# Kernel optimization log

Hardware: AMD Instinct MI355X
Metric: run time of the kernel (lower is better)

The kernel has to match this reference:

```python
import jax, jax.numpy as jnp
import numpy as np

B, M, GRID = 4, 8192, 32          # batches, points per batch, voxel grid side
N = B * M
K = 8                              # knn neighbors (includes self at dist 0)
C_IN, C_OUT, H = 8, 8, 128
KEYB = 64                          # hash base (coords shifted +1 stay in [0,33])
EPS = 1e-5


def setup_inputs() -> dict:
    rng = np.random.default_rng(0)
    # unique occupied voxels per batch (ME SparseTensor requires unique coords)
    cs = []
    for b in range(B):
        lin = rng.choice(GRID ** 3, size=M, replace=False)
        x, y, z = lin // (GRID * GRID), (lin // GRID) % GRID, lin % GRID
        cs.append(np.stack([np.full(M, b), x, y, z], axis=1))
    coords = jnp.asarray(np.concatenate(cs, axis=0).astype(np.int32))  # [N,4]

    key = jax.random.key(0)
    ks = jax.random.split(key, 4)
    feats = jax.random.normal(ks[0], (N, C_IN), jnp.float32)
    w1 = jax.random.normal(ks[1], ((K + 1) * C_IN, H), jnp.float32) * 0.05  # 1x1 conv
    g1 = jnp.ones((H,), jnp.float32)
    b1 = jnp.zeros((H,), jnp.float32)
    w3 = jax.random.normal(ks[2], (27, H, H), jnp.float32) * 0.02          # 3^3 sparse conv
    g2 = jnp.ones((H,), jnp.float32)
    b2 = jnp.zeros((H,), jnp.float32)
    w_out = jax.random.normal(ks[3], (H, 2 * C_OUT), jnp.float32) * 0.05   # 1x1 conv
    return dict(coords=coords, feats=feats, w1=w1, g1=g1, b1=b1,
                w3=w3, g2=g2, b2=b2, w_out=w_out)


def _knn_idx(coords):
    # per-batch brute-force kNN on xyz (batch column segments the search)
    xyz = coords[:, 1:].astype(jnp.float32).reshape(B, M, 3)
    d2 = jnp.sum((xyz[:, :, None, :] - xyz[:, None, :, :]) ** 2, -1)  # [B,M,M]
    _, idx = jax.lax.top_k(-d2, K)                                     # [B,M,K]
    return (idx + (jnp.arange(B) * M)[:, None, None]).reshape(N, K)


def _bn(x, g, b):
    mu = jnp.mean(x, axis=0)
    var = jnp.var(x, axis=0)
    return (x - mu) * jax.lax.rsqrt(var + EPS) * g + b


def reference(coords, feats, w1, g1, b1, w3, g2, b2, w_out):
    # --- kNN gather-and-build: [center || k neighbor feats] -> (k+1)*C_in ---
    nbr = _knn_idx(coords)                                        # [N,K] int
    combined = jnp.concatenate([feats[:, None, :], feats[nbr]], axis=1)
    combined = combined.reshape(N, (K + 1) * C_IN)
    # --- neighbor_processor: 1x1 conv + BN + ReLU ---
    h = jax.nn.relu(_bn(combined @ w1, g1, b1))                   # [N,H]
    # --- context_predictor conv k=3: gather inputs at coord+offset via hash ---
    c = coords[:, 1:] + 1                                         # shift so offsets stay >= 0
    keys = ((coords[:, 0] * KEYB + c[:, 0]) * KEYB + c[:, 1]) * KEYB + c[:, 2]
    order = jnp.argsort(keys)
    skeys = keys[order]
    offs = jnp.stack(jnp.meshgrid(*([jnp.arange(-1, 2)] * 3), indexing='ij'),
                     axis=-1).reshape(27, 3)                      # {-1,0,1}^3
    okey = (offs[:, 0] * KEYB + offs[:, 1]) * KEYB + offs[:, 2]   # [27]
    q = keys[None, :] + okey[:, None]                             # [27,N]
    pos = jnp.clip(jnp.searchsorted(skeys, q), 0, N - 1)
    valid = skeys[pos] == q                                       # [27,N]
    j = order[pos]                                                # [27,N]
    gathered = jnp.where(valid[..., None], h[j], 0.0)             # [27,N,H]
    h2 = jnp.einsum('onc,ocd->nd', gathered, w3)                  # [N,H]
    h2 = jax.nn.relu(_bn(h2, g2, b2))
    # --- final 1x1 conv -> mean/scale ---
    return h2 @ w_out                                             # [N, 2*C_OUT]
```

## Files before the change

kernel.cpp:

```cpp
#include <hip/hip_runtime.h>
#include <hip/hip_bf16.h>

#define B_   4
#define M_   8192
#define N_   32768
#define H_   128
#define EPS_ 1e-5f
#define TBL  1048576
#define GUARD 8192

typedef short short8 __attribute__((ext_vector_type(8)));
typedef float f32x4  __attribute__((ext_vector_type(4)));

__global__ __launch_bounds__(256) void prep_kernel(const int* __restrict__ coords,
                                                   int* __restrict__ table,
                                                   int* __restrict__ packed,
                                                   int* __restrict__ keyb,
                                                   float* __restrict__ gsum,
                                                   unsigned int* __restrict__ hbz) {
    int n = blockIdx.x * 256 + threadIdx.x;
    int b = coords[4*n+0], x = coords[4*n+1], y = coords[4*n+2], z = coords[4*n+3];
    packed[n] = (x << 10) | (y << 5) | z;
    int key = ((b*64 + x+1)*64 + y+1)*64 + (z+1);
    keyb[n] = key;
    table[key] = n;
    if (blockIdx.x == 0) gsum[threadIdx.x] = 0.f;
    if (blockIdx.x == 1 && threadIdx.x < 64) hbz[threadIdx.x] = 0u;
}

__global__ __launch_bounds__(256) void w3pack_kernel(const float* __restrict__ w3,
                                                     ushort* __restrict__ w3f) {
    int t = blockIdx.x * 256 + threadIdx.x;
    int lane = t & 63;
    int ct   = (t >> 6) & 7;
    int ks   = (t >> 9) & 3;
    int o    = t >> 11;
    int quad = lane >> 4, l15 = lane & 15;
    int n = ct*16 + l15;
    const float* src = w3 + o*16384;
    ushort out8[8];
#pragma unroll
    for (int j = 0; j < 8; ++j) {
        int c = ks*32 + quad*8 + j;
        float v = src[c*128 + n];
        __hip_bfloat16 bv = __float2bfloat16(v);
        ushort u; __builtin_memcpy(&u, &bv, 2);
        out8[j] = u;
    }
    *(uint4*)&w3f[t*8] = *(uint4*)out8;
}

__global__ __launch_bounds__(256) void knn_window_kernel(const int* __restrict__ table,
                                                         const int* __restrict__ keyb,
                                                         int* __restrict__ nbr,
                                                         int* __restrict__ flagcnt,
                                                         int* __restrict__ flaglist) {
    __shared__ int okey_sh[125], d2_sh[125];
    __shared__ int tops[256 * 8];
    int tid = threadIdx.x;
    if (tid < 125) {
        int dx = tid / 25 - 2, rr = tid % 25, dy = rr / 5 - 2, dz = rr % 5 - 2;
        okey_sh[tid] = dx * 4096 + dy * 64 + dz;
        d2_sh[tid]   = dx*dx + dy*dy + dz*dz;
    }
    __syncthreads();

    int q   = blockIdx.x * 64 + (tid >> 2);
    int sub = tid & 3;
    int kb  = keyb[q];

    int top[8];
#pragma unroll
    for (int k = 0; k < 8; ++k) top[k] = 0x7FFFFFFF;

    int base = sub * 32;
    int cnt  = (sub == 3) ? 29 : 32;
    for (int i = 0; i < cnt; ++i) {
        int idx = base + i;
        int j = table[kb + okey_sh[idx]];
        if (j >= 0) {
            int key = (d2_sh[idx] << 13) | (j & 8191);
            if (key < top[7]) {
#pragma unroll
                for (int k = 7; k >= 1; --k)
                    top[k] = (key < top[k]) ? max(key, top[k-1]) : top[k];
                top[0] = min(key, top[0]);
            }
        }
    }
#pragma unroll
    for (int k = 0; k < 8; ++k) tops[tid*8 + k] = top[k];
    __syncthreads();

    if (sub == 0) {
        const int* L = &tops[tid*8];
        int ia0 = 0, ia1 = 0, ia2 = 0, ia3 = 0;
        int res[8];
#pragma unroll
        for (int k = 0; k < 8; ++k) {
            int v0 = L[ia0], v1 = L[8 + ia1], v2 = L[16 + ia2], v3 = L[24 + ia3];
            int m01 = min(v0, v1), m23 = min(v2, v3);
            int m = min(m01, m23);
            res[k] = m;
            if (m == v0) ++ia0; else if (m == v1) ++ia1;
            else if (m == v2) ++ia2; else ++ia3;
        }
        int bb = q & ~(M_-1);
        if ((res[7] >> 13) <= 8) {
#pragma unroll
            for (int k = 0; k < 8; ++k) nbr[q*8 + k] = bb + (res[k] & 8191);
        } else {
            int pos = atomicAdd(flagcnt, 1);
            flaglist[pos] = q;
        }
    }
}

__global__ __launch_bounds__(256) void knn_bf_kernel(const int* __restrict__ packed,
                                                     const int* __restrict__ flagcnt,
                                                     const int* __restrict__ flaglist,
                                                     int* __restrict__ nbr) {
    __shared__ int tops[256 * 8];
    int tid = threadIdx.x;
    int cnt = *flagcnt;
    for (int f = blockIdx.x; f < cnt; f += gridDim.x) {
        int n = flaglist[f];
        int bb = n & ~(M_-1);
        int p = packed[n];
        int qx = (p >> 10) & 31, qy = (p >> 5) & 31, qz = p & 31;
        int top[8];
#pragma unroll
        for (int k = 0; k < 8; ++k) top[k] = 0x7FFFFFFF;
        for (int j = tid; j < M_; j += 256) {
            int c = packed[bb + j];
            int dx = qx - ((c >> 10) & 31);
            int dy = qy - ((c >> 5) & 31);
            int dz = qz - (c & 31);
            int d2 = dx*dx + dy*dy + dz*dz;
            int key = (d2 << 13) | j;
            if (key < top[7]) {
#pragma unroll
                for (int k = 7; k >= 1; --k)
                    top[k] = (key < top[k]) ? max(key, top[k-1]) : top[k];
                top[0] = min(key, top[0]);
            }
        }
#pragma unroll
        for (int k = 0; k < 8; ++k) tops[tid*8 + k] = top[k];
        __syncthreads();
        for (int stride = 128; stride >= 1; stride >>= 1) {
            if (tid < stride) {
                int* A  = &tops[tid*8];
                int* Bp = &tops[(tid+stride)*8];
                int r[8]; int ia = 0, ib = 0;
#pragma unroll
                for (int k = 0; k < 8; ++k) {
                    int a = A[ia], b2 = Bp[ib];
                    if (a <= b2) { r[k] = a; ++ia; } else { r[k] = b2; ++ib; }
                }
#pragma unroll
                for (int k = 0; k < 8; ++k) A[k] = r[k];
            }
            __syncthreads();
        }
        if (tid == 0) {
#pragma unroll
            for (int k = 0; k < 8; ++k) nbr[n*8 + k] = bb + (tops[k] & 8191);
        }
        __syncthreads();
    }
}

__global__ __launch_bounds__(256) void h1_kernel(const float* __restrict__ feats,
                                                 const int* __restrict__ nbr,
                                                 const float* __restrict__ w1,
                                                 float* __restrict__ hpre) {
    __shared__ float comb[16][72];
    int tid = threadIdx.x;
    int rowbase = blockIdx.x * 16;
    if (tid < 144) {
        int r = tid / 9, s = tid % 9;
        int grow = rowbase + r;
        int idx = (s == 0) ? grow : nbr[grow*8 + (s-1)];
        const float4* f = (const float4*)(feats + idx * 8);
        float4 a = f[0], b = f[1];
        float* dp = &comb[r][s*8];
        dp[0]=a.x; dp[1]=a.y; dp[2]=a.z; dp[3]=a.w;
        dp[4]=b.x; dp[5]=b.y; dp[6]=b.z; dp[7]=b.w;
    }
    __syncthreads();
    int c = tid & 127, rh = tid >> 7;
    float acc[8];
#pragma unroll
    for (int i = 0; i < 8; ++i) acc[i] = 0.f;
    for (int s = 0; s < 72; ++s) {
        float w = w1[s*128 + c];
#pragma unroll
        for (int i = 0; i < 8; ++i)
            acc[i] += comb[rh*8 + i][s] * w;
    }
#pragma unroll
    for (int i = 0; i < 8; ++i)
        hpre[(rowbase + rh*8 + i)*128 + c] = acc[i];
}

__global__ __launch_bounds__(256) void reduce_kernel(const float* __restrict__ src,
                                                     float* __restrict__ part) {
    __shared__ float ssum[256], ssq[256];
    int tid = threadIdx.x;
    int c = tid & 127, halfr = tid >> 7;
    int rowbase = blockIdx.x * 128 + halfr * 64;
    float s = 0.f, q = 0.f;
    for (int i = 0; i < 64; ++i) {
        float v = src[(rowbase + i)*128 + c];
        s += v; q += v*v;
    }
    ssum[tid] = s; ssq[tid] = q;
    __syncthreads();
    if (tid < 128) {
        part[blockIdx.x*256 + tid]       = ssum[tid] + ssum[tid+128];
        part[blockIdx.x*256 + 128 + tid] = ssq[tid]  + ssq[tid+128];
    }
}

__global__ __launch_bounds__(128) void stats_kernel(const float* __restrict__ part,
                                                    const float* __restrict__ g,
                                                    const float* __restrict__ bias,
                                                    float* __restrict__ scale,
                                                    float* __restrict__ shift) {
    int c = threadIdx.x;
    float s = 0.f, q = 0.f;
    for (int b = 0; b < 256; ++b) {
        s += part[b*256 + c];
        q += part[b*256 + 128 + c];
    }
    float mu  = s / (float)N_;
    float var = q / (float)N_ - mu*mu;
    float inv = rsqrtf(var + EPS_);
    float sc  = inv * g[c];
    scale[c] = sc;
    shift[c] = bias[c] - mu * sc;
}

__global__ __launch_bounds__(128) void stats2_kernel(const float* __restrict__ gsum,
                                                     const float* __restrict__ g,
                                                     const float* __restrict__ bias,
                                                     float* __restrict__ scale,
                                                     float* __restrict__ shift) {
    int c = threadIdx.x;
    float s = gsum[c], q = gsum[128 + c];
    float mu  = s / (float)N_;
    float var = q / (float)N_ - mu*mu;
    float inv = rsqrtf(var + EPS_);
    float sc  = inv * g[c];
    scale[c] = sc;
    shift[c] = bias[c] - mu * sc;
}

__global__ __launch_bounds__(256) void bnrelu_bf16_kernel(const float* __restrict__ x,
                                                          const float* __restrict__ scale,
                                                          const float* __restrict__ shift,
                                                          ushort* __restrict__ y) {
    int i = blockIdx.x * 256 + threadIdx.x;
    float4 v = ((const float4*)x)[i];
    int c = (i * 4) & 127;
    v.x = fmaxf(0.f, v.x*scale[c]   + shift[c]);
    v.y = fmaxf(0.f, v.y*scale[c+1] + shift[c+1]);
    v.z = fmaxf(0.f, v.z*scale[c+2] + shift[c+2]);
    v.w = fmaxf(0.f, v.w*scale[c+3] + shift[c+3]);
    ushort o[4];
#pragma unroll
    for (int k = 0; k < 4; ++k) {
        float f = (&v.x)[k];
        __hip_bfloat16 bv = __float2bfloat16(f);
        __builtin_memcpy(&o[k], &bv, 2);
    }
    ((ushort4*)y)[i] = make_ushort4(o[0], o[1], o[2], o[3]);
}

#define CONV3_LDS 145408
__global__ __launch_bounds__(512) void conv3_mfma_kernel(const ushort* __restrict__ hb,
                                                         const ushort* __restrict__ w3f,
                                                         const int* __restrict__ table,
                                                         const int* __restrict__ keyb,
                                                         float* __restrict__ h2,
                                                         float* __restrict__ gsum) {
    extern __shared__ char smem_raw[];
    ushort* Asb = (ushort*)smem_raw;
    ushort* Bsb = (ushort*)(smem_raw + 65536);
    int*    jsh = (int*)(smem_raw + 131072);
    int*    kbsh= (int*)(smem_raw + 144896);

    int tid = threadIdx.x;
    int lane = tid & 63, wid = tid >> 6;
    int quad = lane >> 4, l15 = lane & 15;
    int bid = blockIdx.x;
    int swz = (bid & 7) * 32 + (bid >> 3);
    int rowbase = swz * 128;
    int wr = wid >> 1;
    int cb = (wid & 1) * 4;

    if (tid < 128) kbsh[tid] = keyb[rowbase + tid];
    __syncthreads();
    for (int t = tid; t < 27*128; t += 512) {
        int o = t >> 7, r = t & 127;
        int dx = o/9 - 1, dy = (o/3)%3 - 1, dz = o%3 - 1;
        jsh[t] = table[kbsh[r] + dx*4096 + dy*64 + dz];
    }
    __syncthreads();

#pragma unroll
    for (int i = 0; i < 4; ++i) {
        int flat = i*512 + tid;
        int r = flat >> 4, cp = flat & 15;
        int j = jsh[r];
        const ushort* asrc = hb + j*128 + ((cp ^ (r & 15)) << 3);
        __builtin_amdgcn_global_load_lds(
            (const __attribute__((address_space(1))) unsigned int*)asrc,
            (__attribute__((address_space(3))) unsigned int*)&Asb[flat << 3],
            16, 0, 0);
        __builtin_amdgcn_global_load_lds(
            (const __attribute__((address_space(1))) unsigned int*)(w3f + (flat << 3)),
            (__attribute__((address_space(3))) unsigned int*)&Bsb[flat << 3],
            16, 0, 0);
    }
    __syncthreads();

    f32x4 acc[2][4];
#pragma unroll
    for (int i = 0; i < 2; ++i)
#pragma unroll
        for (int c = 0; c < 4; ++c)
            acc[i][c] = (f32x4){0.f, 0.f, 0.f, 0.f};

    int cur = 0;
#pragma unroll 1
    for (int o = 0; o < 27; ++o) {
        if (o < 26) {
            int obase = (o + 1) << 7;
            const ushort* wsrc = w3f + ((o + 1) << 14);
            int dst = (cur ^ 1) * 16384;
#pragma unroll
            for (int i = 0; i < 4; ++i) {
                int flat = i*512 + tid;
                int r = flat >> 4, cp = flat & 15;
                int j = jsh[obase + r];
                const ushort* asrc = hb + j*128 + ((cp ^ (r & 15)) << 3);
                __builtin_amdgcn_global_load_lds(
                    (const __attribute__((address_space(1))) unsigned int*)asrc,
                    (__attribute__((address_space(3))) unsigned int*)&Asb[dst + (flat << 3)],
                    16, 0, 0);
                __builtin_amdgcn_global_load_lds(
                    (const __attribute__((address_space(1))) unsigned int*)(wsrc + (flat << 3)),
                    (__attribute__((address_space(3))) unsigned int*)&Bsb[dst + (flat << 3)],
                    16, 0, 0);
            }
        }
        const ushort* Ac = Asb + cur*16384;
        const ushort* Bc = Bsb + cur*16384;
#pragma unroll
        for (int ks = 0; ks < 4; ++ks) {
            short8 af[2], bfr[4];
#pragma unroll
            for (int i = 0; i < 2; ++i) {
                int lr = wr*32 + i*16 + l15;
                int chunk = (ks*4 + quad) ^ l15;
                af[i] = *(const short8*)&Ac[lr*128 + chunk*8];
            }
#pragma unroll
            for (int c = 0; c < 4; ++c)
                bfr[c] = *(const short8*)&Bc[((ks*8 + cb + c)*64 + lane) << 3];
#pragma unroll
            for (int i = 0; i < 2; ++i)
#pragma unroll
                for (int c = 0; c < 4; ++c)
                    acc[i][c] = __builtin_amdgcn_mfma_f32_16x16x32_bf16(af[i], bfr[c], acc[i][c], 0, 0, 0);
        }
        __syncthreads();
        cur ^= 1;
    }

    float s[4], q[4];
#pragma unroll
    for (int c = 0; c < 4; ++c) { s[c] = 0.f; q[c] = 0.f; }
#pragma unroll
    for (int i = 0; i < 2; ++i)
#pragma unroll
        for (int c = 0; c < 4; ++c)
#pragma unroll
            for (int r = 0; r < 4; ++r) {
                int row = rowbase + wr*32 + i*16 + quad*4 + r;
                int col = (cb + c)*16 + l15;
                float v = acc[i][c][r];
                h2[row*128 + col] = v;
                s[c] += v; q[c] += v*v;
            }
    float* red = (float*)smem_raw;
    if (tid < 256) red[tid] = 0.f;
    __syncthreads();
#pragma unroll
    for (int c = 0; c < 4; ++c) {
        int col = (cb + c)*16 + l15;
        atomicAdd(&red[col], s[c]);
        atomicAdd(&red[128 + col], q[c]);
    }
    __syncthreads();
    if (tid < 256) atomicAdd(&gsum[tid], red[tid]);
}

__global__ __launch_bounds__(256) void out_kernel(const float* __restrict__ h2,
                                                  const float* __restrict__ wout,
                                                  const float* __restrict__ scale,
                                                  const float* __restrict__ shift,
                                                  float* __restrict__ out) {
    __shared__ float sc[128], sh[128];
    int tid = threadIdx.x;
    if (tid < 128) { sc[tid] = scale[tid]; sh[tid] = shift[tid]; }
    __syncthreads();
    int r = tid >> 4, d = tid & 15;
    int row = blockIdx.x * 16 + r;
    float acc = 0.f;
    for (int c = 0; c < 128; ++c) {
        float hv = fmaxf(0.f, fmaf(h2[row*128 + c], sc[c], sh[c]));
        acc = fmaf(hv, wout[c*16 + d], acc);
    }
    out[row*16 + d] = acc;
}

extern "C" void kernel_launch(void* const* d_in, const int* in_sizes, int n_in,
                              void* d_out, int out_size, void* d_ws, size_t ws_size,
                              hipStream_t stream) {
    const int*   coords = (const int*)d_in[0];
    const float* feats  = (const float*)d_in[1];
    const float* w1     = (const float*)d_in[2];
    const float* g1     = (const float*)d_in[3];
    const float* b1     = (const float*)d_in[4];
    const float* w3     = (const float*)d_in[5];
    const float* g2     = (const float*)d_in[6];
    const float* b2     = (const float*)d_in[7];
    const float* wout   = (const float*)d_in[8];
    float* out = (float*)d_out;

    char* ws = (char*)d_ws;
    int*    table_base = (int*)(ws);
    int*    table   = table_base + GUARD;
    int*    packed  = (int*)(ws + (4352u<<10));
    int*    keyb    = (int*)(ws + (4608u<<10));
    int*    nbr     = (int*)(ws + (4864u<<10));
    int*    flagcnt = (int*)(ws + (5888u<<10));
    int*    flaglist= (int*)(ws + (5892u<<10));
    float*  part    = (float*)(ws + (6144u<<10));
    float*  scale1  = (float*)(ws + (6400u<<10));
    float*  shift1  = scale1 + 128;
    float*  scale2  = shift1 + 128;
    float*  shift2  = scale2 + 128;
    float*  gsum    = (float*)(ws + (6416u<<10));
    ushort* w3f     = (ushort*)(ws + (6656u<<10));
    ushort* hb      = (ushort*)(ws + (7680u<<10));
    float*  h       = (float*)(ws + (15872u<<10));
    float*  h2      = h;

    static bool conv3_attr_set = false;
    if (!conv3_attr_set) {
        hipFuncSetAttribute(reinterpret_cast<const void*>(&conv3_mfma_kernel),
                            hipFuncAttributeMaxDynamicSharedMemorySize, CONV3_LDS);
        conv3_attr_set = true;
    }

    hipMemsetAsync(table_base, 0xFF, (TBL + GUARD) * sizeof(int), stream);
    hipMemsetAsync(flagcnt, 0, sizeof(int), stream);
    prep_kernel      <<<N_/256, 256, 0, stream>>>(coords, table, packed, keyb,
                                                  gsum, (unsigned int*)(hb - 128));
    w3pack_kernel    <<<216, 256, 0, stream>>>(w3, w3f);
    knn_window_kernel<<<N_/64, 256, 0, stream>>>(table, keyb, nbr, flagcnt, flaglist);
    knn_bf_kernel    <<<256, 256, 0, stream>>>(packed, flagcnt, flaglist, nbr);
    h1_kernel        <<<N_/16, 256, 0, stream>>>(feats, nbr, w1, h);
    reduce_kernel    <<<N_/128, 256, 0, stream>>>(h, part);
    stats_kernel     <<<1, 128, 0, stream>>>(part, g1, b1, scale1, shift1);
    bnrelu_bf16_kernel<<<(N_*H_/4)/256, 256, 0, stream>>>(h, scale1, shift1, hb);
    conv3_mfma_kernel<<<N_/128, 512, CONV3_LDS, stream>>>(hb, w3f, table, keyb, h2, gsum);
    stats2_kernel    <<<1, 128, 0, stream>>>(gsum, g2, b2, scale2, shift2);
    out_kernel       <<<N_/16, 256, 0, stream>>>(h2, wout, scale2, shift2, out);
}
```

Before: 228.4 us.

## Fuse BN statistics into producers, merge prep kernels, prune kNN window

Merges prep and w3 packing into one launch and moves the flag-counter reset there, replacing a memset. BN1 sum and sum-of-squares are now accumulated in h1_kernel with atomics into 8 slots, so the separate reduce pass over h disappears. The stats kernels are folded into bnrelu and out_kernel, which each recompute scale and shift per block. The kNN window now probes only offsets with squared distance at most 8 instead of the full 5x5x5 cube. out_kernel is rebuilt to stage 128 rows and the output weights in LDS with vectorised loads. These changes cut launches and an extra full read of h. The cost is atomic contention, redundant per-block stats work, and kNN correctness resting on the brute-force fallback catching points the smaller window misses.

```diff
diff --git a/kernel.cpp b/kernel.cpp
--- a/kernel.cpp
+++ b/kernel.cpp
@@ -12,25 +12,31 @@
 typedef short short8 __attribute__((ext_vector_type(8)));
 typedef float f32x4  __attribute__((ext_vector_type(4)));
 
-__global__ __launch_bounds__(256) void prep_kernel(const int* __restrict__ coords,
-                                                   int* __restrict__ table,
-                                                   int* __restrict__ packed,
-                                                   int* __restrict__ keyb,
-                                                   float* __restrict__ gsum,
-                                                   unsigned int* __restrict__ hbz) {
-    int n = blockIdx.x * 256 + threadIdx.x;
-    int b = coords[4*n+0], x = coords[4*n+1], y = coords[4*n+2], z = coords[4*n+3];
-    packed[n] = (x << 10) | (y << 5) | z;
-    int key = ((b*64 + x+1)*64 + y+1)*64 + (z+1);
-    keyb[n] = key;
-    table[key] = n;
-    if (blockIdx.x == 0) gsum[threadIdx.x] = 0.f;
-    if (blockIdx.x == 1 && threadIdx.x < 64) hbz[threadIdx.x] = 0u;
-}
-
-__global__ __launch_bounds__(256) void w3pack_kernel(const float* __restrict__ w3,
-                                                     ushort* __restrict__ w3f) {
-    int t = blockIdx.x * 256 + threadIdx.x;
+__global__ __launch_bounds__(256) void prep_pack_kernel(const int* __restrict__ coords,
+                                                        int* __restrict__ table,
+                                                        int* __restrict__ packed,
+                                                        int* __restrict__ keyb,
+                                                        const float* __restrict__ w3,
+                                                        ushort* __restrict__ w3f,
+                                                        float* __restrict__ gsum1,
+                                                        float* __restrict__ gsum2,
+                                                        int* __restrict__ flagcnt,
+                                                        unsigned int* __restrict__ hbz) {
+    int bid = blockIdx.x, tid = threadIdx.x;
+    if (bid < 128) {
+        int n = bid * 256 + tid;
+        int b = coords[4*n+0], x = coords[4*n+1], y = coords[4*n+2], z = coords[4*n+3];
+        packed[n] = (x << 10) | (y << 5) | z;
+        int key = ((b*64 + x+1)*64 + y+1)*64 + (z+1);
+        keyb[n] = key;
+        table[key] = n;
+        if (bid < 8)  gsum1[bid*256 + tid] = 0.f;
+        if (bid == 0) gsum2[tid] = 0.f;
+        if (bid == 8 && tid < 64) hbz[tid] = 0u;
+        if (bid == 9 && tid == 0) *flagcnt = 0;
+        return;
+    }
+    int t = (bid - 128) * 256 + tid;
     int lane = t & 63;
     int ct   = (t >> 6) & 7;
     int ks   = (t >> 9) & 3;
@@ -55,13 +61,20 @@
                                                          int* __restrict__ nbr,
                                                          int* __restrict__ flagcnt,
                                                          int* __restrict__ flaglist) {
-    __shared__ int okey_sh[125], d2_sh[125];
+    __shared__ int okey_sh[93], d2_sh[93];
     __shared__ int tops[256 * 8];
+    __shared__ int ncnt;
     int tid = threadIdx.x;
+    if (tid == 0) ncnt = 0;
+    __syncthreads();
     if (tid < 125) {
         int dx = tid / 25 - 2, rr = tid % 25, dy = rr / 5 - 2, dz = rr % 5 - 2;
-        okey_sh[tid] = dx * 4096 + dy * 64 + dz;
-        d2_sh[tid]   = dx*dx + dy*dy + dz*dz;
+        int d2 = dx*dx + dy*dy + dz*dz;
+        if (d2 <= 8) {
+            int p = atomicAdd(&ncnt, 1);
+            okey_sh[p] = dx * 4096 + dy * 64 + dz;
+            d2_sh[p]   = d2;
+        }
     }
     __syncthreads();
 
@@ -73,8 +86,8 @@
 #pragma unroll
     for (int k = 0; k < 8; ++k) top[k] = 0x7FFFFFFF;
 
-    int base = sub * 32;
-    int cnt  = (sub == 3) ? 29 : 32;
+    int base = sub * 24;
+    int cnt  = (sub == 3) ? 21 : 24;
     for (int i = 0; i < cnt; ++i) {
         int idx = base + i;
         int j = table[kb + okey_sh[idx]];
@@ -174,8 +187,10 @@
 __global__ __launch_bounds__(256) void h1_kernel(const float* __restrict__ feats,
                                                  const int* __restrict__ nbr,
                                                  const float* __restrict__ w1,
-                                                 float* __restrict__ hpre) {
+                                                 float* __restrict__ hpre,
+                                                 float* __restrict__ gsum1) {
     __shared__ float comb[16][72];
+    __shared__ float ssum[256], ssq[256];
     int tid = threadIdx.x;
     int rowbase = blockIdx.x * 16;
     if (tid < 144) {
@@ -199,75 +214,52 @@
         for (int i = 0; i < 8; ++i)
             acc[i] += comb[rh*8 + i][s] * w;
     }
-#pragma unroll
-    for (int i = 0; i < 8; ++i)
+    float s = 0.f, q = 0.f;
+#pragma unroll
+    for (int i = 0; i < 8; ++i) {
         hpre[(rowbase + rh*8 + i)*128 + c] = acc[i];
-}
-
-__global__ __launch_bounds__(256) void reduce_kernel(const float* __restrict__ src,
-                                                     float* __restrict__ part) {
-    __shared__ float ssum[256], ssq[256];
+        s += acc[i]; q += acc[i]*acc[i];
+    }
+    ssum[tid] = s; ssq[tid] = q;
+    __syncthreads();
+    if (tid < 128) {
+        float S = ssum[tid] + ssum[tid+128];
+        float Q = ssq[tid]  + ssq[tid+128];
+        float* g = gsum1 + (blockIdx.x & 7) * 256;
+        atomicAdd(&g[tid], S);
+        atomicAdd(&g[128 + tid], Q);
+    }
+}
+
+__global__ __launch_bounds__(256) void bnrelu_bf16_kernel(const float* __restrict__ x,
+                                                          const float* __restrict__ gsum1,
+                                                          const float* __restrict__ g1,
+                                                          const float* __restrict__ b1,
+                                                          ushort* __restrict__ y) {
+    __shared__ float sc[128], sh[128];
     int tid = threadIdx.x;
-    int c = tid & 127, halfr = tid >> 7;
-    int rowbase = blockIdx.x * 128 + halfr * 64;
-    float s = 0.f, q = 0.f;
-    for (int i = 0; i < 64; ++i) {
-        float v = src[(rowbase + i)*128 + c];
-        s += v; q += v*v;
-    }
-    ssum[tid] = s; ssq[tid] = q;
-    __syncthreads();
     if (tid < 128) {
-        part[blockIdx.x*256 + tid]       = ssum[tid] + ssum[tid+128];
-        part[blockIdx.x*256 + 128 + tid] = ssq[tid]  + ssq[tid+128];
-    }
-}
-
-__global__ __launch_bounds__(128) void stats_kernel(const float* __restrict__ part,
-                                                    const float* __restrict__ g,
-                                                    const float* __restrict__ bias,
-                                                    float* __restrict__ scale,
-                                                    float* __restrict__ shift) {
-    int c = threadIdx.x;
-    float s = 0.f, q = 0.f;
-    for (int b = 0; b < 256; ++b) {
-        s += part[b*256 + c];
-        q += part[b*256 + 128 + c];
-    }
-    float mu  = s / (float)N_;
-    float var = q / (float)N_ - mu*mu;
-    float inv = rsqrtf(var + EPS_);
-    float sc  = inv * g[c];
-    scale[c] = sc;
-    shift[c] = bias[c] - mu * sc;
-}
-
-__global__ __launch_bounds__(128) void stats2_kernel(const float* __restrict__ gsum,
-                                                     const float* __restrict__ g,
-                                                     const float* __restrict__ bias,
-                                                     float* __restrict__ scale,
-                                                     float* __restrict__ shift) {
-    int c = threadIdx.x;
-    float s = gsum[c], q = gsum[128 + c];
-    float mu  = s / (float)N_;
-    float var = q / (float)N_ - mu*mu;
-    float inv = rsqrtf(var + EPS_);
-    float sc  = inv * g[c];
-    scale[c] = sc;
-    shift[c] = bias[c] - mu * sc;
-}
-
-__global__ __launch_bounds__(256) void bnrelu_bf16_kernel(const float* __restrict__ x,
-                                                          const float* __restrict__ scale,
-                                                          const float* __restrict__ shift,
-                                                          ushort* __restrict__ y) {
-    int i = blockIdx.x * 256 + threadIdx.x;
+        float s = 0.f, q = 0.f;
+#pragma unroll
+        for (int r = 0; r < 8; ++r) {
+            s += gsum1[r*256 + tid];
+            q += gsum1[r*256 + 128 + tid];
+        }
+        float mu  = s / (float)N_;
+        float var = q / (float)N_ - mu*mu;
+        float inv = rsqrtf(var + EPS_);
+        float scv = inv * g1[tid];
+        sc[tid] = scv;
+        sh[tid] = b1[tid] - mu * scv;
+    }
+    __syncthreads();
+    int i = blockIdx.x * 256 + tid;
     float4 v = ((const float4*)x)[i];
     int c = (i * 4) & 127;
-    v.x = fmaxf(0.f, v.x*scale[c]   + shift[c]);
-    v.y = fmaxf(0.f, v.y*scale[c+1] + shift[c+1]);
-    v.z = fmaxf(0.f, v.z*scale[c+2] + shift[c+2]);
-    v.w = fmaxf(0.f, v.w*scale[c+3] + shift[c+3]);
+    v.x = fmaxf(0.f, v.x*sc[c]   + sh[c]);
+    v.y = fmaxf(0.f, v.y*sc[c+1] + sh[c+1]);
+    v.z = fmaxf(0.f, v.z*sc[c+2] + sh[c+2]);
+    v.w = fmaxf(0.f, v.w*sc[c+3] + sh[c+3]);
     ushort o[4];
 #pragma unroll
     for (int k = 0; k < 4; ++k) {
@@ -410,21 +402,62 @@
 
 __global__ __launch_bounds__(256) void out_kernel(const float* __restrict__ h2,
                                                   const float* __restrict__ wout,
-                                                  const float* __restrict__ scale,
-                                                  const float* __restrict__ shift,
+                                                  const float* __restrict__ gsum2,
+                                                  const float* __restrict__ g2,
+                                                  const float* __restrict__ b2,
                                                   float* __restrict__ out) {
+    __shared__ float hrow[128][129];
+    __shared__ float wsh[2048];
     __shared__ float sc[128], sh[128];
     int tid = threadIdx.x;
-    if (tid < 128) { sc[tid] = scale[tid]; sh[tid] = shift[tid]; }
-    __syncthreads();
-    int r = tid >> 4, d = tid & 15;
-    int row = blockIdx.x * 16 + r;
-    float acc = 0.f;
+    if (tid < 128) {
+        float s = gsum2[tid], q = gsum2[128 + tid];
+        float mu  = s / (float)N_;
+        float var = q / (float)N_ - mu*mu;
+        float inv = rsqrtf(var + EPS_);
+        float scv = inv * g2[tid];
+        sc[tid] = scv;
+        sh[tid] = b2[tid] - mu * scv;
+    }
+#pragma unroll
+    for (int i = 0; i < 8; ++i) wsh[i*256 + tid] = wout[i*256 + tid];
+    __syncthreads();
+
+    int rowbase = blockIdx.x * 128;
+#pragma unroll
+    for (int i = 0; i < 16; ++i) {
+        int flat = i*256 + tid;
+        int row = flat >> 5, c4 = (flat & 31) * 4;
+        float4 v = *(const float4*)&h2[(rowbase + row)*128 + c4];
+        float4 scv = *(const float4*)&sc[c4];
+        float4 shv = *(const float4*)&sh[c4];
+        hrow[row][c4+0] = fmaxf(0.f, fmaf(v.x, scv.x, shv.x));
+        hrow[row][c4+1] = fmaxf(0.f, fmaf(v.y, scv.y, shv.y));
+        hrow[row][c4+2] = fmaxf(0.f, fmaf(v.z, scv.z, shv.z));
+        hrow[row][c4+3] = fmaxf(0.f, fmaf(v.w, scv.w, shv.w));
+    }
+    __syncthreads();
+
+    int row = tid >> 1, dbase = (tid & 1) * 8;
+    float acc[8];
+#pragma unroll
+    for (int k = 0; k < 8; ++k) acc[k] = 0.f;
     for (int c = 0; c < 128; ++c) {
-        float hv = fmaxf(0.f, fmaf(h2[row*128 + c], sc[c], sh[c]));
-        acc = fmaf(hv, wout[c*16 + d], acc);
-    }
-    out[row*16 + d] = acc;
+        float hv = hrow[row][c];
+        float4 w0 = *(const float4*)&wsh[c*16 + dbase];
+        float4 w1 = *(const float4*)&wsh[c*16 + dbase + 4];
+        acc[0] = fmaf(hv, w0.x, acc[0]);
+        acc[1] = fmaf(hv, w0.y, acc[1]);
+        acc[2] = fmaf(hv, w0.z, acc[2]);
+        acc[3] = fmaf(hv, w0.w, acc[3]);
+        acc[4] = fmaf(hv, w1.x, acc[4]);
+        acc[5] = fmaf(hv, w1.y, acc[5]);
+        acc[6] = fmaf(hv, w1.z, acc[6]);
+        acc[7] = fmaf(hv, w1.w, acc[7]);
+    }
+    float* op = out + (rowbase + row)*16 + dbase;
+    *(float4*)op       = (float4){acc[0], acc[1], acc[2], acc[3]};
+    *(float4*)(op + 4) = (float4){acc[4], acc[5], acc[6], acc[7]};
 }
 
 extern "C" void kernel_launch(void* const* d_in, const int* in_sizes, int n_in,
@@ -449,12 +482,8 @@
     int*    nbr     = (int*)(ws + (4864u<<10));
     int*    flagcnt = (int*)(ws + (5888u<<10));
     int*    flaglist= (int*)(ws + (5892u<<10));
-    float*  part    = (float*)(ws + (6144u<<10));
-    float*  scale1  = (float*)(ws + (6400u<<10));
-    float*  shift1  = scale1 + 128;
-    float*  scale2  = shift1 + 128;
-    float*  shift2  = scale2 + 128;
-    float*  gsum    = (float*)(ws + (6416u<<10));
+    float*  gsum2   = (float*)(ws + (6416u<<10));
+    float*  gsum1   = (float*)(ws + (6420u<<10));
     ushort* w3f     = (ushort*)(ws + (6656u<<10));
     ushort* hb      = (ushort*)(ws + (7680u<<10));
     float*  h       = (float*)(ws + (15872u<<10));
@@ -468,17 +497,13 @@
     }
 
     hipMemsetAsync(table_base, 0xFF, (TBL + GUARD) * sizeof(int), stream);
-    hipMemsetAsync(flagcnt, 0, sizeof(int), stream);
-    prep_kernel      <<<N_/256, 256, 0, stream>>>(coords, table, packed, keyb,
-                                                  gsum, (unsigned int*)(hb - 128));
-    w3pack_kernel    <<<216, 256, 0, stream>>>(w3, w3f);
+    prep_pack_kernel <<<344, 256, 0, stream>>>(coords, table, packed, keyb, w3, w3f,
+                                               gsum1, gsum2, flagcnt,
+                                               (unsigned int*)(hb - 128));
     knn_window_kernel<<<N_/64, 256, 0, stream>>>(table, keyb, nbr, flagcnt, flaglist);
     knn_bf_kernel    <<<256, 256, 0, stream>>>(packed, flagcnt, flaglist, nbr);
-    h1_kernel        <<<N_/16, 256, 0, stream>>>(feats, nbr, w1, h);
-    reduce_kernel    <<<N_/128, 256, 0, stream>>>(h, part);
-    stats_kernel     <<<1, 128, 0, stream>>>(part, g1, b1, scale1, shift1);
-    bnrelu_bf16_kernel<<<(N_*H_/4)/256, 256, 0, stream>>>(h, scale1, shift1, hb);
-    conv3_mfma_kernel<<<N_/128, 512, CONV3_LDS, stream>>>(hb, w3f, table, keyb, h2, gsum);
-    stats2_kernel    <<<1, 128, 0, stream>>>(gsum, g2, b2, scale2, shift2);
-    out_kernel       <<<N_/16, 256, 0, stream>>>(h2, wout, scale2, shift2, out);
-}
+    h1_kernel        <<<N_/16, 256, 0, stream>>>(feats, nbr, w1, h, gsum1);
+    bnrelu_bf16_kernel<<<(N_*H_/4)/256, 256, 0, stream>>>(h, gsum1, g1, b1, hb);
+    conv3_mfma_kernel<<<N_/128, 512, CONV3_LDS, stream>>>(hb, w3f, table, keyb, h2, gsum2);
+    out_kernel       <<<N_/128, 256, 0, stream>>>(h2, wout, gsum2, g2, b2, out);
+}
```

New measurement: 194.3 us. -14.9%, faster.
